# Kernel tuning notes

Measured on AMD Instinct MI355X. Metric: run time of the kernel, lower is better.

## Reference

```python
import jax, jax.numpy as jnp
import numpy as np

N_NODES = 100000
N_EDGES = 3200000
IN_FEATURES = 128
OUT_FEATURES = 32


def setup_inputs() -> dict:
    key = jax.random.key(0)
    k_x, k_w, k_src, k_dst, k_ew = jax.random.split(key, 5)
    x = jax.random.normal(k_x, (N_NODES, IN_FEATURES), dtype=jnp.float32)
    W = jax.random.normal(k_w, (IN_FEATURES, OUT_FEATURES), dtype=jnp.float32) * (1.0 / np.sqrt(IN_FEATURES))
    edge_src = jax.random.randint(k_src, (N_EDGES,), 0, N_NODES, dtype=jnp.int32)
    edge_dst = jax.random.randint(k_dst, (N_EDGES,), 0, N_NODES, dtype=jnp.int32)
    edge_weight = jax.random.uniform(k_ew, (N_EDGES,), dtype=jnp.float32)
    return {"x": x, "W": W, "edge_src": edge_src, "edge_dst": edge_dst, "edge_weight": edge_weight}


def reference(x, W, edge_src, edge_dst, edge_weight):
    # GCNConv.forward: h = linear(x) (no bias), then out = sparse.mm(A_hat, h)
    h = x @ W                                   # [N, out]
    # SpMM as gather -> weight -> segment-sum over destination nodes.
    msgs = edge_weight[:, None] * h[edge_src]   # [E, out]
    out = jax.ops.segment_sum(msgs, edge_dst, num_segments=N_NODES)  # [N, out]
    return out
```

## Files before the change

kernel.cpp:

```cpp
#include <hip/hip_runtime.h>
#include <hip/hip_bf16.h>

#define IN_F 128
#define OUT_F 32
#define BSHIFT 7
#define NPB 128
#define BCHUNK 4096
#define BIN_THREADS 1024
#define GAT_THREADS 512
#define TILE 2048
#define MAXBIN 1024
#define CAP 5120

static __device__ inline unsigned short f2bf_rne(float f) {
    unsigned u = __float_as_uint(f);
    unsigned r = u + 0x7FFF + ((u >> 16) & 1);
    return (unsigned short)(r >> 16);
}

__global__ void gcn_gemm_h(const float* __restrict__ x, const float* __restrict__ W,
                           unsigned short* __restrict__ h, int n_rows)
{
    __shared__ float Wl[IN_F * OUT_F];
    const int tid = threadIdx.x;
    const float4* W4 = (const float4*)W;
    float4* Wl4 = (float4*)Wl;
    #pragma unroll
    for (int i = 0; i < 4; ++i)
        Wl4[tid + i * 256] = W4[tid + i * 256];
    __syncthreads();

    const int c4   = tid & 7;
    const int rloc = tid >> 3;
    const int row  = blockIdx.x * 32 + rloc;
    if (row >= n_rows) return;

    const float4* xr = (const float4*)(x + (size_t)row * IN_F);
    float4 acc = {0.f, 0.f, 0.f, 0.f};
    #pragma unroll
    for (int k4 = 0; k4 < IN_F / 4; ++k4) {
        const float4 xv = xr[k4];
        #pragma unroll
        for (int j = 0; j < 4; ++j) {
            const int k = k4 * 4 + j;
            const float4 wv = *(const float4*)(&Wl[k * OUT_F + c4 * 4]);
            const float xs = (&xv.x)[j];
            acc.x += xs * wv.x;
            acc.y += xs * wv.y;
            acc.z += xs * wv.z;
            acc.w += xs * wv.w;
        }
    }
    ushort4 o = { f2bf_rne(acc.x), f2bf_rne(acc.y), f2bf_rne(acc.z), f2bf_rne(acc.w) };
    *(ushort4*)(&h[(size_t)row * OUT_F + c4 * 4]) = o;
}

__global__ __launch_bounds__(1024)
void gcn_initcur(int* __restrict__ gcur, int nb)
{
    const int i = blockIdx.x * 1024 + threadIdx.x;
    if (i < nb) gcur[i] = i * CAP;
}

__global__ __launch_bounds__(BIN_THREADS)
void gcn_bin(const int* __restrict__ esrc, const int* __restrict__ edst,
             const float* __restrict__ ew, int* __restrict__ gcur,
             int2* __restrict__ recs, int n_edges, int nb)
{
    __shared__ int2 sorted[BCHUNK];
    __shared__ unsigned short binOf[BCHUNK];
    __shared__ int hist[MAXBIN];
    __shared__ int cursor[MAXBIN];
    __shared__ int gbase[MAXBIN];
    __shared__ int wpart[16];
    __shared__ int wpre[16];

    const int tid = threadIdx.x;
    const int k   = blockIdx.x;
    const int base  = k * BCHUNK;
    const int count = min(BCHUNK, n_edges - base);

    for (int i = tid; i < nb; i += BIN_THREADS) hist[i] = 0;
    __syncthreads();
    for (int i = tid; i < count; i += BIN_THREADS)
        atomicAdd(&hist[edst[base + i] >> BSHIFT], 1);
    __syncthreads();

    const int v = (tid < nb) ? hist[tid] : 0;
    int sc = v;
    #pragma unroll
    for (int off = 1; off < 64; off <<= 1) {
        const int t = __shfl_up(sc, off, 64);
        if ((tid & 63) >= off) sc += t;
    }
    if ((tid & 63) == 63) wpart[tid >> 6] = sc;
    __syncthreads();
    if (tid < 16) {
        const int pv = wpart[tid];
        int ps = pv;
        #pragma unroll
        for (int off = 1; off < 16; off <<= 1) {
            const int t = __shfl_up(ps, off, 64);
            if (tid >= off) ps += t;
        }
        wpre[tid] = ps - pv;
    }
    __syncthreads();
    if (tid < nb) {
        const int beg = sc - v + wpre[tid >> 6];
        cursor[tid] = beg;
        int gb = 0;
        if (v > 0) gb = atomicAdd(&gcur[tid], v);
        gbase[tid] = gb - beg;
    }
    __syncthreads();

    for (int i = tid; i < count; i += BIN_THREADS) {
        const int e = base + i;
        const int d = edst[e];
        const int bk = d >> BSHIFT;
        const int pos = atomicAdd(&cursor[bk], 1);
        sorted[pos] = make_int2(esrc[e] | ((d & (NPB - 1)) << 17), __float_as_int(ew[e]));
        binOf[pos]  = (unsigned short)bk;
    }
    __syncthreads();

    for (int i = tid; i < count; i += BIN_THREADS)
        recs[gbase[binOf[i]] + i] = sorted[i];
}

__global__ __launch_bounds__(GAT_THREADS)
void gcn_sort_gather(const unsigned short* __restrict__ h,
                     const int2* __restrict__ recs,
                     const int* __restrict__ gcur,
                     float* __restrict__ out, int n_nodes)
{
    __shared__ int2 sbuf[TILE];
    __shared__ int2 sorted[TILE];
    __shared__ int hist[NPB];
    __shared__ int nbeg[NPB];
    __shared__ int cursor[NPB];
    __shared__ int wpart[2];

    const int b   = blockIdx.x;
    const int tid = threadIdx.x;
    const int s   = b * CAP;
    const int cnt = gcur[b] - s;
    const int grp = tid >> 4;
    const int c2  = tid & 15;

    float accx[4] = {0.f, 0.f, 0.f, 0.f};
    float accy[4] = {0.f, 0.f, 0.f, 0.f};

    for (int t0 = 0; t0 < cnt; t0 += TILE) {
        const int tc = min(TILE, cnt - t0);
        __syncthreads();
        if (tid < NPB) hist[tid] = 0;
        __syncthreads();
        for (int i = tid; i < tc; i += GAT_THREADS) {
            const int2 r = recs[s + t0 + i];
            sbuf[i] = r;
            atomicAdd(&hist[(r.x >> 17) & (NPB - 1)], 1);
        }
        __syncthreads();

        const int v = (tid < NPB) ? hist[tid] : 0;
        int sc = v;
        #pragma unroll
        for (int off = 1; off < 64; off <<= 1) {
            const int t = __shfl_up(sc, off, 64);
            if ((tid & 63) >= off) sc += t;
        }
        if (tid < NPB && (tid & 63) == 63) wpart[tid >> 6] = sc;
        __syncthreads();
        if (tid < NPB) {
            const int beg = sc - v + ((tid >= 64) ? wpart[0] : 0);
            nbeg[tid]   = beg;
            cursor[tid] = beg;
        }
        __syncthreads();

        for (int i = tid; i < tc; i += GAT_THREADS) {
            const int2 r = sbuf[i];
            const int pos = atomicAdd(&cursor[(r.x >> 17) & (NPB - 1)], 1);
            sorted[pos] = r;
        }
        __syncthreads();

        #pragma unroll
        for (int n = 0; n < 4; ++n) {
            const int dL = (grp << 2) + n;
            int i = nbeg[dL];
            const int e = i + hist[dL];
            float ax = 0.f, ay = 0.f;
            for (; i + 4 <= e; i += 4) {
                const int2 r0 = sorted[i];
                const int2 r1 = sorted[i + 1];
                const int2 r2 = sorted[i + 2];
                const int2 r3 = sorted[i + 3];
                const unsigned v0 = *(const unsigned*)(h + ((size_t)(r0.x & 0x1FFFF) << 5) + (c2 << 1));
                const unsigned v1 = *(const unsigned*)(h + ((size_t)(r1.x & 0x1FFFF) << 5) + (c2 << 1));
                const unsigned v2 = *(const unsigned*)(h + ((size_t)(r2.x & 0x1FFFF) << 5) + (c2 << 1));
                const unsigned v3 = *(const unsigned*)(h + ((size_t)(r3.x & 0x1FFFF) << 5) + (c2 << 1));
                const float w0 = __int_as_float(r0.y);
                const float w1 = __int_as_float(r1.y);
                const float w2 = __int_as_float(r2.y);
                const float w3 = __int_as_float(r3.y);
                ax += w0 * __uint_as_float(v0 << 16);
                ay += w0 * __uint_as_float(v0 & 0xFFFF0000u);
                ax += w1 * __uint_as_float(v1 << 16);
                ay += w1 * __uint_as_float(v1 & 0xFFFF0000u);
                ax += w2 * __uint_as_float(v2 << 16);
                ay += w2 * __uint_as_float(v2 & 0xFFFF0000u);
                ax += w3 * __uint_as_float(v3 << 16);
                ay += w3 * __uint_as_float(v3 & 0xFFFF0000u);
            }
            for (; i < e; ++i) {
                const int2 r = sorted[i];
                const unsigned hv = *(const unsigned*)(h + ((size_t)(r.x & 0x1FFFF) << 5) + (c2 << 1));
                const float w = __int_as_float(r.y);
                ax += w * __uint_as_float(hv << 16);
                ay += w * __uint_as_float(hv & 0xFFFF0000u);
            }
            accx[n] += ax;
            accy[n] += ay;
        }
    }

    const int nodeBase = b << BSHIFT;
    #pragma unroll
    for (int n = 0; n < 4; ++n) {
        const int node = nodeBase + (grp << 2) + n;
        if (node < n_nodes) {
            float2 o = { accx[n], accy[n] };
            *(float2*)(out + ((size_t)node << 5) + (c2 << 1)) = o;
        }
    }
}

__global__ void gcn_fused_fallback(const float* __restrict__ x, const float* __restrict__ W,
                                   const int* __restrict__ esrc,
                                   const int* __restrict__ edst,
                                   const float* __restrict__ ew,
                                   float* __restrict__ out,
                                   long long total_units)
{
    __shared__ float Wl[IN_F * OUT_F];
    const int tid = threadIdx.x;
    const float4* W4 = (const float4*)W;
    float4* Wl4 = (float4*)Wl;
    #pragma unroll
    for (int i = 0; i < 4; ++i)
        Wl4[tid + i * 256] = W4[tid + i * 256];
    __syncthreads();

    long long u = (long long)blockIdx.x * blockDim.x + threadIdx.x;
    if (u >= total_units) return;
    const int e = (int)(u >> 5);
    const int c = (int)(u & 31);
    const int s  = esrc[e];
    const int d  = edst[e];
    const float w = ew[e];

    const float4* xr = (const float4*)(x + (size_t)s * IN_F);
    float acc = 0.f;
    #pragma unroll
    for (int k4 = 0; k4 < IN_F / 4; ++k4) {
        const float4 xv = xr[k4];
        acc += xv.x * Wl[(k4 * 4 + 0) * OUT_F + c];
        acc += xv.y * Wl[(k4 * 4 + 1) * OUT_F + c];
        acc += xv.z * Wl[(k4 * 4 + 2) * OUT_F + c];
        acc += xv.w * Wl[(k4 * 4 + 3) * OUT_F + c];
    }
    atomicAdd(out + (size_t)d * OUT_F + c, w * acc);
}

static inline size_t align_up(size_t v, size_t a) { return (v + a - 1) & ~(a - 1); }

extern "C" void kernel_launch(void* const* d_in, const int* in_sizes, int n_in,
                              void* d_out, int out_size, void* d_ws, size_t ws_size,
                              hipStream_t stream)
{
    const float* x  = (const float*)d_in[0];
    const float* W  = (const float*)d_in[1];
    const int* esrc = (const int*)d_in[2];
    const int* edst = (const int*)d_in[3];
    const float* ew = (const float*)d_in[4];
    float* out = (float*)d_out;

    const int n_nodes = in_sizes[0] / IN_F;
    const int n_edges = in_sizes[2];

    const int nb       = (n_nodes + NPB - 1) >> BSHIFT;
    const int n_chunks = (n_edges + BCHUNK - 1) / BCHUNK;
    const int avg_per_bucket = n_edges / nb;

    const size_t h_bytes    = align_up((size_t)n_nodes * OUT_F * sizeof(unsigned short), 256);
    const size_t cur_bytes  = align_up((size_t)nb * sizeof(int), 256);
    const size_t recs_bytes = align_up((size_t)nb * CAP * sizeof(int2) + 16, 256);
    const size_t need = h_bytes + cur_bytes + recs_bytes;

    if (ws_size >= need && nb <= MAXBIN && avg_per_bucket + 16 * 64 < CAP) {
        char* p = (char*)d_ws;
        unsigned short* h = (unsigned short*)p;  p += h_bytes;
        int* gcur     = (int*)p;                 p += cur_bytes;
        int2* recs    = (int2*)p;

        const int gemm_blocks = (n_nodes + 31) / 32;
        gcn_gemm_h<<<gemm_blocks, 256, 0, stream>>>(x, W, h, n_nodes);

        gcn_initcur<<<(nb + 1023) / 1024, 1024, 0, stream>>>(gcur, nb);
        gcn_bin<<<n_chunks, BIN_THREADS, 0, stream>>>(esrc, edst, ew, gcur,
                                                      recs, n_edges, nb);
        gcn_sort_gather<<<nb, GAT_THREADS, 0, stream>>>(h, recs, gcur, out, n_nodes);
    } else {
        hipMemsetAsync(d_out, 0, (size_t)out_size * sizeof(float), stream);
        const long long total_units = (long long)n_edges * 32;
        const int fblocks = (int)((total_units + 255) / 256);
        gcn_fused_fallback<<<fblocks, 256, 0, stream>>>(x, W, esrc, edst, ew, out, total_units);
    }
}
```

Baseline: 98.82 us.

## Fuse GEMM and edge binning into one launch, replace cursor init with memset

The separate GEMM and binning kernels become one kernel that dispatches on block index: the first n_chunks blocks bin edges and the rest compute h with 128 rows per 1024-thread block. The cursor-init kernel is replaced by a memset, and cursors now hold relative counts with the bucket base added in the bin and gather kernels. This cuts one launch and lets the GEMM and binning work run side by side on the GPU. The cost is one shared-memory size sized for the larger binning layout, which may limit how many GEMM blocks fit per CU.

New measurement: 99.89 us. About the same (+1.1%).

```diff
diff --git a/kernel.cpp b/kernel.cpp
--- a/kernel.cpp
+++ b/kernel.cpp
@@ -6,7 +6,7 @@
 #define BSHIFT 7
 #define NPB 128
 #define BCHUNK 4096
-#define BIN_THREADS 1024
+#define FUSED_THREADS 1024
 #define GAT_THREADS 512
 #define TILE 2048
 #define MAXBIN 1024
@@ -18,71 +18,63 @@
     return (unsigned short)(r >> 16);
 }
 
-__global__ void gcn_gemm_h(const float* __restrict__ x, const float* __restrict__ W,
-                           unsigned short* __restrict__ h, int n_rows)
+__global__ __launch_bounds__(FUSED_THREADS)
+void gcn_gemm_bin(const float* __restrict__ x, const float* __restrict__ W,
+                  unsigned short* __restrict__ h, int n_rows,
+                  const int* __restrict__ esrc, const int* __restrict__ edst,
+                  const float* __restrict__ ew, int* __restrict__ gcur,
+                  int2* __restrict__ recs, int n_edges, int nb, int n_chunks)
 {
-    __shared__ float Wl[IN_F * OUT_F];
+    extern __shared__ char smem[];
     const int tid = threadIdx.x;
-    const float4* W4 = (const float4*)W;
-    float4* Wl4 = (float4*)Wl;
-    #pragma unroll
-    for (int i = 0; i < 4; ++i)
-        Wl4[tid + i * 256] = W4[tid + i * 256];
-    __syncthreads();
-
-    const int c4   = tid & 7;
-    const int rloc = tid >> 3;
-    const int row  = blockIdx.x * 32 + rloc;
-    if (row >= n_rows) return;
-
-    const float4* xr = (const float4*)(x + (size_t)row * IN_F);
-    float4 acc = {0.f, 0.f, 0.f, 0.f};
-    #pragma unroll
-    for (int k4 = 0; k4 < IN_F / 4; ++k4) {
-        const float4 xv = xr[k4];
+
+    if ((int)blockIdx.x >= n_chunks) {
+        float* Wl = (float*)smem;
+        const float4* W4 = (const float4*)W;
+        ((float4*)Wl)[tid] = W4[tid];
+        __syncthreads();
+
+        const int c4   = tid & 7;
+        const int rloc = tid >> 3;
+        const int row  = ((int)blockIdx.x - n_chunks) * 128 + rloc;
+        if (row >= n_rows) return;
+
+        const float4* xr = (const float4*)(x + (size_t)row * IN_F);
+        float4 acc = {0.f, 0.f, 0.f, 0.f};
         #pragma unroll
-        for (int j = 0; j < 4; ++j) {
-            const int k = k4 * 4 + j;
-            const float4 wv = *(const float4*)(&Wl[k * OUT_F + c4 * 4]);
-            const float xs = (&xv.x)[j];
-            acc.x += xs * wv.x;
-            acc.y += xs * wv.y;
-            acc.z += xs * wv.z;
-            acc.w += xs * wv.w;
-        }
-    }
-    ushort4 o = { f2bf_rne(acc.x), f2bf_rne(acc.y), f2bf_rne(acc.z), f2bf_rne(acc.w) };
-    *(ushort4*)(&h[(size_t)row * OUT_F + c4 * 4]) = o;
-}
-
-__global__ __launch_bounds__(1024)
-void gcn_initcur(int* __restrict__ gcur, int nb)
-{
-    const int i = blockIdx.x * 1024 + threadIdx.x;
-    if (i < nb) gcur[i] = i * CAP;
-}
-
-__global__ __launch_bounds__(BIN_THREADS)
-void gcn_bin(const int* __restrict__ esrc, const int* __restrict__ edst,
-             const float* __restrict__ ew, int* __restrict__ gcur,
-             int2* __restrict__ recs, int n_edges, int nb)
-{
-    __shared__ int2 sorted[BCHUNK];
-    __shared__ unsigned short binOf[BCHUNK];
-    __shared__ int hist[MAXBIN];
-    __shared__ int cursor[MAXBIN];
-    __shared__ int gbase[MAXBIN];
-    __shared__ int wpart[16];
-    __shared__ int wpre[16];
-
-    const int tid = threadIdx.x;
+        for (int k4 = 0; k4 < IN_F / 4; ++k4) {
+            const float4 xv = xr[k4];
+            #pragma unroll
+            for (int j = 0; j < 4; ++j) {
+                const int k = k4 * 4 + j;
+                const float4 wv = *(const float4*)(&Wl[k * OUT_F + c4 * 4]);
+                const float xs = (&xv.x)[j];
+                acc.x += xs * wv.x;
+                acc.y += xs * wv.y;
+                acc.z += xs * wv.z;
+                acc.w += xs * wv.w;
+            }
+        }
+        ushort4 o = { f2bf_rne(acc.x), f2bf_rne(acc.y), f2bf_rne(acc.z), f2bf_rne(acc.w) };
+        *(ushort4*)(&h[(size_t)row * OUT_F + c4 * 4]) = o;
+        return;
+    }
+
+    int2* sorted = (int2*)smem;
+    int*  hist   = (int*)(smem + BCHUNK * sizeof(int2));
+    int*  cursor = hist + MAXBIN;
+    int*  gbase  = cursor + MAXBIN;
+    int*  wpart  = gbase + MAXBIN;
+    int*  wpre   = wpart + 16;
+    unsigned short* binOf = (unsigned short*)(wpre + 16);
+
     const int k   = blockIdx.x;
     const int base  = k * BCHUNK;
     const int count = min(BCHUNK, n_edges - base);
 
-    for (int i = tid; i < nb; i += BIN_THREADS) hist[i] = 0;
-    __syncthreads();
-    for (int i = tid; i < count; i += BIN_THREADS)
+    for (int i = tid; i < nb; i += FUSED_THREADS) hist[i] = 0;
+    __syncthreads();
+    for (int i = tid; i < count; i += FUSED_THREADS)
         atomicAdd(&hist[edst[base + i] >> BSHIFT], 1);
     __syncthreads();
 
@@ -109,13 +101,13 @@
     if (tid < nb) {
         const int beg = sc - v + wpre[tid >> 6];
         cursor[tid] = beg;
-        int gb = 0;
-        if (v > 0) gb = atomicAdd(&gcur[tid], v);
+        int gb = tid * CAP;
+        if (v > 0) gb += atomicAdd(&gcur[tid], v);
         gbase[tid] = gb - beg;
     }
     __syncthreads();
 
-    for (int i = tid; i < count; i += BIN_THREADS) {
+    for (int i = tid; i < count; i += FUSED_THREADS) {
         const int e = base + i;
         const int d = edst[e];
         const int bk = d >> BSHIFT;
@@ -125,7 +117,7 @@
     }
     __syncthreads();
 
-    for (int i = tid; i < count; i += BIN_THREADS)
+    for (int i = tid; i < count; i += FUSED_THREADS)
         recs[gbase[binOf[i]] + i] = sorted[i];
 }
 
@@ -145,9 +137,10 @@
     const int b   = blockIdx.x;
     const int tid = threadIdx.x;
     const int s   = b * CAP;
-    const int cnt = gcur[b] - s;
+    const int cnt = gcur[b];
     const int grp = tid >> 4;
     const int c2  = tid & 15;
+    const size_t hoff = (size_t)(c2 << 1);
 
     float accx[4] = {0.f, 0.f, 0.f, 0.f};
     float accy[4] = {0.f, 0.f, 0.f, 0.f};
@@ -198,10 +191,10 @@
                 const int2 r1 = sorted[i + 1];
                 const int2 r2 = sorted[i + 2];
                 const int2 r3 = sorted[i + 3];
-                const unsigned v0 = *(const unsigned*)(h + ((size_t)(r0.x & 0x1FFFF) << 5) + (c2 << 1));
-                const unsigned v1 = *(const unsigned*)(h + ((size_t)(r1.x & 0x1FFFF) << 5) + (c2 << 1));
-                const unsigned v2 = *(const unsigned*)(h + ((size_t)(r2.x & 0x1FFFF) << 5) + (c2 << 1));
-                const unsigned v3 = *(const unsigned*)(h + ((size_t)(r3.x & 0x1FFFF) << 5) + (c2 << 1));
+                const unsigned v0 = *(const unsigned*)(h + (((size_t)(r0.x & 0x1FFFF)) << 5) + hoff);
+                const unsigned v1 = *(const unsigned*)(h + (((size_t)(r1.x & 0x1FFFF)) << 5) + hoff);
+                const unsigned v2 = *(const unsigned*)(h + (((size_t)(r2.x & 0x1FFFF)) << 5) + hoff);
+                const unsigned v3 = *(const unsigned*)(h + (((size_t)(r3.x & 0x1FFFF)) << 5) + hoff);
                 const float w0 = __int_as_float(r0.y);
                 const float w1 = __int_as_float(r1.y);
                 const float w2 = __int_as_float(r2.y);
@@ -217,7 +210,7 @@
             }
             for (; i < e; ++i) {
                 const int2 r = sorted[i];
-                const unsigned hv = *(const unsigned*)(h + ((size_t)(r.x & 0x1FFFF) << 5) + (c2 << 1));
+                const unsigned hv = *(const unsigned*)(h + (((size_t)(r.x & 0x1FFFF)) << 5) + hoff);
                 const float w = __int_as_float(r.y);
                 ax += w * __uint_as_float(hv << 16);
                 ay += w * __uint_as_float(hv & 0xFFFF0000u);
@@ -293,12 +286,18 @@
 
     const int nb       = (n_nodes + NPB - 1) >> BSHIFT;
     const int n_chunks = (n_edges + BCHUNK - 1) / BCHUNK;
+    const int gemm_blocks = (n_nodes + 127) / 128;
     const int avg_per_bucket = n_edges / nb;
 
     const size_t h_bytes    = align_up((size_t)n_nodes * OUT_F * sizeof(unsigned short), 256);
     const size_t cur_bytes  = align_up((size_t)nb * sizeof(int), 256);
     const size_t recs_bytes = align_up((size_t)nb * CAP * sizeof(int2) + 16, 256);
     const size_t need = h_bytes + cur_bytes + recs_bytes;
+
+    const size_t bin_smem  = BCHUNK * sizeof(int2) + (3 * MAXBIN + 32) * sizeof(int)
+                           + BCHUNK * sizeof(unsigned short);
+    const size_t gemm_smem = (size_t)IN_F * OUT_F * sizeof(float);
+    const size_t smem = bin_smem > gemm_smem ? bin_smem : gemm_smem;
 
     if (ws_size >= need && nb <= MAXBIN && avg_per_bucket + 16 * 64 < CAP) {
         char* p = (char*)d_ws;
@@ -306,12 +305,11 @@
         int* gcur     = (int*)p;                 p += cur_bytes;
         int2* recs    = (int2*)p;
 
-        const int gemm_blocks = (n_nodes + 31) / 32;
-        gcn_gemm_h<<<gemm_blocks, 256, 0, stream>>>(x, W, h, n_nodes);
-
-        gcn_initcur<<<(nb + 1023) / 1024, 1024, 0, stream>>>(gcur, nb);
-        gcn_bin<<<n_chunks, BIN_THREADS, 0, stream>>>(esrc, edst, ew, gcur,
-                                                      recs, n_edges, nb);
+        hipMemsetAsync(gcur, 0, (size_t)nb * sizeof(int), stream);
+
+        gcn_gemm_bin<<<n_chunks + gemm_blocks, FUSED_THREADS, smem, stream>>>(
+            x, W, h, n_nodes, esrc, edst, ew, gcur, recs, n_edges, nb, n_chunks);
+
         gcn_sort_gather<<<nb, GAT_THREADS, 0, stream>>>(h, recs, gcur, out, n_nodes);
     } else {
         hipMemsetAsync(d_out, 0, (size_t)out_size * sizeof(float), stream);
```

## Remap gather threads to one node per 4 threads with 16-byte loads

Applied to the files above, without the earlier changes.

Changes the gather stage's thread mapping. Each destination node is now handled by 4 threads instead of 16, and each thread loads 16 bytes (8 bf16 features) per edge instead of 4 bytes, accumulating 8 floats. The aim is fewer, wider memory instructions and a single sequential edge walk per thread instead of 4 per-node loops. In exchange, edge-list reads from shared memory are spread over more groups, more accumulator registers are used, and load imbalance between nodes with different degrees now lands within a wavefront.

Result: faster. 93.94 us (-4.9%).

```diff
diff --git a/kernel.cpp b/kernel.cpp
--- a/kernel.cpp
+++ b/kernel.cpp
@@ -146,11 +146,12 @@
     const int tid = threadIdx.x;
     const int s   = b * CAP;
     const int cnt = gcur[b] - s;
-    const int grp = tid >> 4;
-    const int c2  = tid & 15;
-
-    float accx[4] = {0.f, 0.f, 0.f, 0.f};
-    float accy[4] = {0.f, 0.f, 0.f, 0.f};
+    const int grp = tid >> 2;
+    const int q   = tid & 3;
+    const size_t hoff = (size_t)(q << 3);
+
+    float a0 = 0.f, a1 = 0.f, a2 = 0.f, a3 = 0.f;
+    float a4 = 0.f, a5 = 0.f, a6 = 0.f, a7 = 0.f;
 
     for (int t0 = 0; t0 < cnt; t0 += TILE) {
         const int tc = min(TILE, cnt - t0);
@@ -187,54 +188,78 @@
         }
         __syncthreads();
 
-        #pragma unroll
-        for (int n = 0; n < 4; ++n) {
-            const int dL = (grp << 2) + n;
-            int i = nbeg[dL];
-            const int e = i + hist[dL];
-            float ax = 0.f, ay = 0.f;
+        {
+            int i = nbeg[grp];
+            const int e = i + hist[grp];
             for (; i + 4 <= e; i += 4) {
                 const int2 r0 = sorted[i];
                 const int2 r1 = sorted[i + 1];
                 const int2 r2 = sorted[i + 2];
                 const int2 r3 = sorted[i + 3];
-                const unsigned v0 = *(const unsigned*)(h + ((size_t)(r0.x & 0x1FFFF) << 5) + (c2 << 1));
-                const unsigned v1 = *(const unsigned*)(h + ((size_t)(r1.x & 0x1FFFF) << 5) + (c2 << 1));
-                const unsigned v2 = *(const unsigned*)(h + ((size_t)(r2.x & 0x1FFFF) << 5) + (c2 << 1));
-                const unsigned v3 = *(const unsigned*)(h + ((size_t)(r3.x & 0x1FFFF) << 5) + (c2 << 1));
+                const uint4 v0 = *(const uint4*)(h + (((size_t)(r0.x & 0x1FFFF)) << 5) + hoff);
+                const uint4 v1 = *(const uint4*)(h + (((size_t)(r1.x & 0x1FFFF)) << 5) + hoff);
+                const uint4 v2 = *(const uint4*)(h + (((size_t)(r2.x & 0x1FFFF)) << 5) + hoff);
+                const uint4 v3 = *(const uint4*)(h + (((size_t)(r3.x & 0x1FFFF)) << 5) + hoff);
                 const float w0 = __int_as_float(r0.y);
                 const float w1 = __int_as_float(r1.y);
                 const float w2 = __int_as_float(r2.y);
                 const float w3 = __int_as_float(r3.y);
-                ax += w0 * __uint_as_float(v0 << 16);
-                ay += w0 * __uint_as_float(v0 & 0xFFFF0000u);
-                ax += w1 * __uint_as_float(v1 << 16);
-                ay += w1 * __uint_as_float(v1 & 0xFFFF0000u);
-                ax += w2 * __uint_as_float(v2 << 16);
-                ay += w2 * __uint_as_float(v2 & 0xFFFF0000u);
-                ax += w3 * __uint_as_float(v3 << 16);
-                ay += w3 * __uint_as_float(v3 & 0xFFFF0000u);
+                a0 += w0 * __uint_as_float(v0.x << 16);
+                a1 += w0 * __uint_as_float(v0.x & 0xFFFF0000u);
+                a2 += w0 * __uint_as_float(v0.y << 16);
+                a3 += w0 * __uint_as_float(v0.y & 0xFFFF0000u);
+                a4 += w0 * __uint_as_float(v0.z << 16);
+                a5 += w0 * __uint_as_float(v0.z & 0xFFFF0000u);
+                a6 += w0 * __uint_as_float(v0.w << 16);
+                a7 += w0 * __uint_as_float(v0.w & 0xFFFF0000u);
+                a0 += w1 * __uint_as_float(v1.x << 16);
+                a1 += w1 * __uint_as_float(v1.x & 0xFFFF0000u);
+                a2 += w1 * __uint_as_float(v1.y << 16);
+                a3 += w1 * __uint_as_float(v1.y & 0xFFFF0000u);
+                a4 += w1 * __uint_as_float(v1.z << 16);
+                a5 += w1 * __uint_as_float(v1.z & 0xFFFF0000u);
+                a6 += w1 * __uint_as_float(v1.w << 16);
+                a7 += w1 * __uint_as_float(v1.w & 0xFFFF0000u);
+                a0 += w2 * __uint_as_float(v2.x << 16);
+                a1 += w2 * __uint_as_float(v2.x & 0xFFFF0000u);
+                a2 += w2 * __uint_as_float(v2.y << 16);
+                a3 += w2 * __uint_as_float(v2.y & 0xFFFF0000u);
+                a4 += w2 * __uint_as_float(v2.z << 16);
+                a5 += w2 * __uint_as_float(v2.z & 0xFFFF0000u);
+                a6 += w2 * __uint_as_float(v2.w << 16);
+                a7 += w2 * __uint_as_float(v2.w & 0xFFFF0000u);
+                a0 += w3 * __uint_as_float(v3.x << 16);
+                a1 += w3 * __uint_as_float(v3.x & 0xFFFF0000u);
+                a2 += w3 * __uint_as_float(v3.y << 16);
+                a3 += w3 * __uint_as_float(v3.y & 0xFFFF0000u);
+                a4 += w3 * __uint_as_float(v3.z << 16);
+                a5 += w3 * __uint_as_float(v3.z & 0xFFFF0000u);
+                a6 += w3 * __uint_as_float(v3.w << 16);
+                a7 += w3 * __uint_as_float(v3.w & 0xFFFF0000u);
             }
             for (; i < e; ++i) {
                 const int2 r = sorted[i];
-                const unsigned hv = *(const unsigned*)(h + ((size_t)(r.x & 0x1FFFF) << 5) + (c2 << 1));
+                const uint4 hv = *(const uint4*)(h + (((size_t)(r.x & 0x1FFFF)) << 5) + hoff);
                 const float w = __int_as_float(r.y);
-                ax += w * __uint_as_float(hv << 16);
-                ay += w * __uint_as_float(hv & 0xFFFF0000u);
+                a0 += w * __uint_as_float(hv.x << 16);
+                a1 += w * __uint_as_float(hv.x & 0xFFFF0000u);
+                a2 += w * __uint_as_float(hv.y << 16);
+                a3 += w * __uint_as_float(hv.y & 0xFFFF0000u);
+                a4 += w * __uint_as_float(hv.z << 16);
+                a5 += w * __uint_as_float(hv.z & 0xFFFF0000u);
+                a6 += w * __uint_as_float(hv.w << 16);
+                a7 += w * __uint_as_float(hv.w & 0xFFFF0000u);
             }
-            accx[n] += ax;
-            accy[n] += ay;
-        }
-    }
-
-    const int nodeBase = b << BSHIFT;
-    #pragma unroll
-    for (int n = 0; n < 4; ++n) {
-        const int node = nodeBase + (grp << 2) + n;
-        if (node < n_nodes) {
-            float2 o = { accx[n], accy[n] };
-            *(float2*)(out + ((size_t)node << 5) + (c2 << 1)) = o;
-        }
+        }
+    }
+
+    const int node = (b << BSHIFT) + grp;
+    if (node < n_nodes) {
+        float* op = out + ((size_t)node << 5) + (q << 3);
+        float4 o0 = { a0, a1, a2, a3 };
+        float4 o1 = { a4, a5, a6, a7 };
+        *(float4*)(op)     = o0;
+        *(float4*)(op + 4) = o1;
     }
 }
 
```
